# Kernel optimization log

Measured on AMD Instinct MI355X. Metric: run time of the kernel, lower is better.

The kernel has to match this reference:

```python
import jax, jax.numpy as jnp
import numpy as np

B, S, DMODEL, NHEAD = 2, 2048, 1024, 16
DK = DMODEL // NHEAD
INITRANGE = 0.1


def setup_inputs() -> dict:
    key = jax.random.key(0)
    kq, kk, kv, kwq, kwk, kwv, kwo = jax.random.split(key, 7)
    unif = lambda k, shape: jax.random.uniform(k, shape, jnp.float32, -INITRANGE, INITRANGE)
    return {
        "Q": jax.random.normal(kq, (B, S, DMODEL), jnp.float32),
        "K": jax.random.normal(kk, (B, S, DMODEL), jnp.float32),
        "V": jax.random.normal(kv, (B, S, DMODEL), jnp.float32),
        "WQ": unif(kwq, (NHEAD, DMODEL, DK)),
        "WK": unif(kwk, (NHEAD, DMODEL, DK)),
        "WV": unif(kwv, (NHEAD, DMODEL, DK)),
        "WO": unif(kwo, (NHEAD * DK, DMODEL)),
    }


def reference(Q, K, V, WQ, WK, WV, WO):
    dk = WQ.shape[-1]
    # per-head projections: [B,S,D] x [H,D,dk] -> [B,H,S,dk]
    Qi = jnp.einsum('bsd,hdk->bhsk', Q, WQ)
    Ki = jnp.einsum('bsd,hdk->bhsk', K, WK)
    Vi = jnp.einsum('bsd,hdk->bhsk', V, WV)
    scale = 1.0 / jnp.sqrt(jnp.asarray(dk, Qi.dtype))
    # full attention matrix [B,H,S,S] (faithful to the hand-rolled module; dropout in eval mode)
    attn = jax.nn.softmax(jnp.einsum('bhsk,bhtk->bhst', Qi, Ki) * scale, axis=-1)
    headi = jnp.einsum('bhst,bhtk->bhsk', attn, Vi)  # [B,H,S,dk]
    b, h, s, _ = headi.shape
    # NOTE: original does a raw reshape of contiguous (B,H,S,dk) -> (B,S,H*dk),
    # which mixes head and sequence axes in memory order. jnp row-major reshape
    # reproduces exactly the same element layout.
    out = headi.reshape(b, s, h * dk) @ WO  # [B,S,DMODEL]
    return out
```

## Files before the change

kernel.cpp:

```cpp
#include <hip/hip_runtime.h>
#include <hip/hip_bf16.h>
#include <stdint.h>

typedef unsigned short u16;
typedef unsigned int u32;
typedef __attribute__((ext_vector_type(4))) float f32x4;
typedef __attribute__((ext_vector_type(16))) float f32x16;
typedef __attribute__((ext_vector_type(8))) short bf16x8;
typedef __attribute__((ext_vector_type(4))) unsigned int u32x4;
typedef __attribute__((ext_vector_type(2))) unsigned int u32x2;

#define DEV __device__ __forceinline__

DEV u16 f2bf(float f) {
  union { float f; uint32_t u; } v; v.f = f;
  uint32_t u = v.u;
  return (u16)((u + 0x7fffu + ((u >> 16) & 1u)) >> 16);
}
DEV float bf2f(u16 h) {
  union { uint32_t u; float f; } v; v.u = ((uint32_t)h) << 16;
  return v.f;
}

DEV u32 cvtpk(float a, float b) {
  u32 r;
  asm("v_cvt_pk_bf16_f32 %0, %1, %2" : "=v"(r) : "v"(a), "v"(b));
  return r;
}

DEV void gload_lds16(const u16* g, u16* l) {
  __builtin_amdgcn_global_load_lds(
      (const __attribute__((address_space(1))) void*)g,
      (__attribute__((address_space(3))) void*)l, 16, 0, 0);
}

__global__ __launch_bounds__(256) void prep_kernel(
    const float* __restrict__ Q, const float* __restrict__ K, const float* __restrict__ V,
    const float* __restrict__ WQ, const float* __restrict__ WK, const float* __restrict__ WV,
    const float* __restrict__ WO,
    u16* __restrict__ Qb, u16* __restrict__ Kb, u16* __restrict__ Vb,
    u16* __restrict__ Wt, u16* __restrict__ Wot) {
  const int i = blockIdx.x * 256 + threadIdx.x;
#pragma unroll
  for (int it = 0; it < 3; ++it) {
    int idx = it * 1048576 + i;
    int which = idx >> 20, j = idx & 1048575;
    const float* src = which == 0 ? Q : (which == 1 ? K : V);
    u16* dst = which == 0 ? Qb : (which == 1 ? Kb : Vb);
    float4 v = ((const float4*)src)[j];
    u32x2 pk;
    pk[0] = (u32)f2bf(v.x) | ((u32)f2bf(v.y) << 16);
    pk[1] = (u32)f2bf(v.z) | ((u32)f2bf(v.w) << 16);
    *(u32x2*)(dst + (size_t)j * 4) = pk;
  }
#pragma unroll
  for (int it = 0; it < 4; ++it) {
    int idx = it * 1048576 + i;
    if (idx < 3145728) {
      int p = idx >> 20, r = idx & 1048575;
      int n = r >> 10, d = r & 1023;
      int h = n >> 6, k = n & 63;
      const float* src = p == 0 ? WQ : (p == 1 ? WK : WV);
      Wt[idx] = f2bf(src[(h * 1024 + d) * 64 + k]);
    } else {
      int j = idx - 3145728;
      int c = j >> 10, k = j & 1023;
      Wot[j] = f2bf(WO[k * 1024 + c]);
    }
  }
}

template <int OUT_BF16>
__global__ __launch_bounds__(256, 2) void gemm_kernel(const u16* __restrict__ A,
                                                      const u16* __restrict__ Bt,
                                                      void* __restrict__ Cout) {
  __shared__ __align__(16) u16 Alds[128 * 64];
  __shared__ __align__(16) u16 Blds[128 * 64];
  const size_t zo = blockIdx.z;
  A += zo * 4194304;
  Bt += zo * 1048576;
  const int tid = threadIdx.x;
  const int l = tid & 63, w = tid >> 6;
  const int wm = w >> 1, wn = w & 1;
  const int tileM = blockIdx.x * 128, tileN = blockIdx.y * 128;
  const int lr = l >> 3, lch = l & 7;

  f32x4 acc[4][4] = {};

  for (int kt = 0; kt < 16; ++kt) {
    const int k0 = kt * 64;
#pragma unroll
    for (int i = 0; i < 4; ++i) {
      int r = i * 32 + w * 8 + lr;
      int sch = lch ^ (r & 7);
      gload_lds16(A + (size_t)(tileM + r) * 1024 + k0 + sch * 8, Alds + i * 2048 + w * 512);
      gload_lds16(Bt + (size_t)(tileN + r) * 1024 + k0 + sch * 8, Blds + i * 2048 + w * 512);
    }
    __syncthreads();
    bf16x8 af[4][2], bfr[4][2];
#pragma unroll
    for (int m = 0; m < 4; ++m) {
#pragma unroll
      for (int kk = 0; kk < 2; ++kk) {
        int row = wm * 64 + m * 16 + (l & 15);
        int ch = ((l >> 4) + kk * 4) ^ (row & 7);
        af[m][kk] = *(const bf16x8*)(Alds + row * 64 + ch * 8);
        int rowb = wn * 64 + m * 16 + (l & 15);
        int chb = ((l >> 4) + kk * 4) ^ (rowb & 7);
        bfr[m][kk] = *(const bf16x8*)(Blds + rowb * 64 + chb * 8);
      }
    }
#pragma unroll
    for (int m = 0; m < 4; ++m)
#pragma unroll
      for (int n = 0; n < 4; ++n)
#pragma unroll
        for (int kk = 0; kk < 2; ++kk)
          acc[m][n] = __builtin_amdgcn_mfma_f32_16x16x32_bf16(af[m][kk], bfr[n][kk], acc[m][n], 0, 0, 0);
    __syncthreads();
  }
#pragma unroll
  for (int m = 0; m < 4; ++m) {
    int row0 = tileM + wm * 64 + m * 16 + ((l >> 4) << 2);
#pragma unroll
    for (int n = 0; n < 4; ++n) {
      int col = tileN + wn * 64 + n * 16 + (l & 15);
#pragma unroll
      for (int q = 0; q < 4; ++q) {
        if (OUT_BF16)
          ((u16*)Cout)[zo * 4194304 + (size_t)(row0 + q) * 1024 + col] = f2bf(acc[m][n][q]);
        else
          ((float*)Cout)[(size_t)(row0 + q) * 1024 + col] = acc[m][n][q];
      }
    }
  }
}

__global__ __launch_bounds__(256) void transposeV_kernel(const u16* __restrict__ Vi,
                                                         u16* __restrict__ Vt) {
  __shared__ __align__(16) u16 tl[64][72];
  const int tid = threadIdx.x;
  const int st = blockIdx.x * 64;
  const int bh = blockIdx.y;
  const int b = bh >> 4, h = bh & 15;
#pragma unroll
  for (int i = 0; i < 2; ++i) {
    int idx = i * 256 + tid;
    int s = idx >> 3, ch = idx & 7;
    const u16* src = Vi + (size_t)(b * 2048 + st + s) * 1024 + h * 64 + ch * 8;
    u32x2 a = *(const u32x2*)src;
    u32x2 bb = *(const u32x2*)(src + 4);
    *(u32x2*)&tl[s][ch * 8] = a;
    *(u32x2*)&tl[s][ch * 8 + 4] = bb;
  }
  __syncthreads();
#pragma unroll
  for (int i = 0; i < 2; ++i) {
    int idx = i * 256 + tid;
    int dk = idx >> 3, ch = idx & 7;
    u32x4 outv;
    u16* tp = (u16*)&outv;
#pragma unroll
    for (int j = 0; j < 8; ++j) tp[j] = tl[ch * 8 + j][dk];
    *(u32x4*)(Vt + ((size_t)bh * 64 + dk) * 2048 + st + ch * 8) = outv;
  }
}

__global__ __launch_bounds__(256, 3) void attn_kernel(const u16* __restrict__ Qi,
                                                      const u16* __restrict__ Ki,
                                                      const u16* __restrict__ Vt,
                                                      u16* __restrict__ Op,
                                                      float* __restrict__ Lp) {
  __shared__ __align__(16) u16 Kl[2][4096];
  __shared__ __align__(16) u16 Vl[2][4096];
  const int tid = threadIdx.x;
  const int l = tid & 63, w = tid >> 6;
  const int lq = l & 31, hi = l >> 5;
  const int lr = l >> 3, lch = l & 7;
  const int dd = blockIdx.x;
  const int orig = (dd & 7) * 128 + (dd >> 3);
  const int bh = orig >> 5;
  const int rem = orig & 31;
  const int qb = rem >> 1, kvh = rem & 1;
  const int b = bh >> 4, h = bh & 15;
  const int qt = qb * 128 + w * 32;
  const int tb = kvh * 1024;

  const u16* Kbase = Ki + (size_t)b * 2048 * 1024 + h * 64;
  const u16* Vbase = Vt + (size_t)bh * 64 * 2048;

  bf16x8 qf[4];
  {
    const u16* qp = Qi + (size_t)(b * 2048 + qt + lq) * 1024 + h * 64 + hi * 8;
#pragma unroll
    for (int s = 0; s < 4; ++s) {
      u32x4 t4 = *(const u32x4*)(qp + s * 16);
      u16* tp = (u16*)&t4;
#pragma unroll
      for (int j = 0; j < 8; ++j) tp[j] = f2bf(bf2f(tp[j]) * 0.1803368867f);
      qf[s] = *(bf16x8*)&t4;
    }
  }

  f32x16 o0 = {}, o1 = {};
  float l_r = 0.f;

  auto STAGE = [&](int bb, int t) {
#pragma unroll
    for (int i = 0; i < 2; ++i) {
      int r = i * 32 + w * 8 + lr;
      int sch = lch ^ (r & 7);
      gload_lds16(Kbase + (size_t)(b ? 0 : 0, (size_t)(tb + t * 64 + r)) * 1024 + sch * 8,
                  Kl[bb] + i * 2048 + w * 512);
      gload_lds16(Vbase + (size_t)r * 2048 + tb + t * 64 + sch * 8,
                  Vl[bb] + i * 2048 + w * 512);
    }
  };

  STAGE(0, 0);

  for (int tile = 0; tile < 16; ++tile) {
    const int cur = tile & 1;
    __syncthreads();
    if (tile + 1 < 16) STAGE(cur ^ 1, tile + 1);
    const u16* kl = Kl[cur];
    const u16* vl = Vl[cur];

    f32x16 s0 = {}, s1 = {};
    __builtin_amdgcn_s_setprio(1);
#pragma unroll
    for (int s = 0; s < 4; ++s) {
      int row = lq, c = s * 2 + hi;
      bf16x8 kf = *(const bf16x8*)(kl + row * 64 + (c ^ (row & 7)) * 8);
      s0 = __builtin_amdgcn_mfma_f32_32x32x16_bf16(kf, qf[s], s0, 0, 0, 0);
    }
#pragma unroll
    for (int s = 0; s < 4; ++s) {
      int row = 32 + lq, c = s * 2 + hi;
      bf16x8 kf = *(const bf16x8*)(kl + row * 64 + (c ^ (row & 7)) * 8);
      s1 = __builtin_amdgcn_mfma_f32_32x32x16_bf16(kf, qf[s], s1, 0, 0, 0);
    }
    __builtin_amdgcn_s_setprio(0);

    float rs = 0.f;
    bf16x8 pa[4];
#pragma unroll
    for (int s4 = 0; s4 < 4; ++s4) {
      const int rb = 8 * (s4 & 1);
      float p[8];
#pragma unroll
      for (int j = 0; j < 8; ++j) {
        float sv = (s4 < 2) ? ((const float*)&s0)[rb + j] : ((const float*)&s1)[rb + j];
        p[j] = exp2f(sv);
        rs += p[j];
      }
      u32 w10 = cvtpk(p[0], p[1]);
      u32 w11 = cvtpk(p[2], p[3]);
      u32 w20 = cvtpk(p[4], p[5]);
      u32 w21 = cvtpk(p[6], p[7]);
      u32 send0 = hi ? w10 : w20, send1 = hi ? w11 : w21;
      u32 recv0 = __shfl_xor(send0, 32, 64);
      u32 recv1 = __shfl_xor(send1, 32, 64);
      u32x4 af;
      af[0] = hi ? recv0 : w10;
      af[1] = hi ? recv1 : w11;
      af[2] = hi ? w20 : recv0;
      af[3] = hi ? w21 : recv1;
      pa[s4] = *(bf16x8*)&af;
    }
    rs += __shfl_xor(rs, 32, 64);
    l_r += rs;

    __builtin_amdgcn_s_setprio(1);
#pragma unroll
    for (int s4 = 0; s4 < 4; ++s4) {
      int rowd = lq, c = s4 * 2 + hi;
      bf16x8 vf = *(const bf16x8*)(vl + rowd * 64 + (c ^ (rowd & 7)) * 8);
      o0 = __builtin_amdgcn_mfma_f32_32x32x16_bf16(pa[s4], vf, o0, 0, 0, 0);
    }
#pragma unroll
    for (int s4 = 0; s4 < 4; ++s4) {
      int rowd = 32 + lq, c = s4 * 2 + hi;
      bf16x8 vf = *(const bf16x8*)(vl + rowd * 64 + (c ^ (rowd & 7)) * 8);
      o1 = __builtin_amdgcn_mfma_f32_32x32x16_bf16(pa[s4], vf, o1, 0, 0, 0);
    }
    __builtin_amdgcn_s_setprio(0);
  }

#pragma unroll
  for (int r = 0; r < 16; ++r) {
    int qr = (r & 3) + 8 * (r >> 2) + 4 * hi;
    u16* hp = Op + (size_t)kvh * 4194304 + ((size_t)bh * 2048 + qt + qr) * 64;
    hp[lq] = f2bf(o0[r]);
    hp[32 + lq] = f2bf(o1[r]);
  }
  if (hi == 0) Lp[(size_t)kvh * 65536 + (size_t)bh * 2048 + qt + lq] = l_r;
}

__global__ __launch_bounds__(256) void combine_kernel(const u16* __restrict__ Op,
                                                      const float* __restrict__ Lp,
                                                      u16* __restrict__ Hd) {
  const int idx = blockIdx.x * 256 + threadIdx.x;
  const int g = idx >> 3, j = idx & 7;
  const float fac = 1.f / (Lp[g] + Lp[65536 + g]);
  const u16* a = Op + (size_t)g * 64 + j * 8;
  const u16* bptr = a + 4194304;
  u32x4 va = *(const u32x4*)a;
  u32x4 vb = *(const u32x4*)bptr;
  const u16* pa = (const u16*)&va;
  const u16* pb = (const u16*)&vb;
  u32x4 outv;
  u16* po = (u16*)&outv;
#pragma unroll
  for (int e = 0; e < 8; ++e) po[e] = f2bf((bf2f(pa[e]) + bf2f(pb[e])) * fac);
  *(u32x4*)(Hd + (size_t)g * 64 + j * 8) = outv;
}

extern "C" void kernel_launch(void* const* d_in, const int* in_sizes, int n_in,
                              void* d_out, int out_size, void* d_ws, size_t ws_size,
                              hipStream_t stream) {
  const float* Q = (const float*)d_in[0];
  const float* K = (const float*)d_in[1];
  const float* V = (const float*)d_in[2];
  const float* WQ = (const float*)d_in[3];
  const float* WK = (const float*)d_in[4];
  const float* WV = (const float*)d_in[5];
  const float* WO = (const float*)d_in[6];
  float* out = (float*)d_out;

  size_t off = 0;
  char* ws = (char*)d_ws;
  auto nxt = [&](size_t n) { void* p = ws + off; off += (n + 255) & ~(size_t)255; return p; };
  u16* Qb = (u16*)nxt(3ull * 4096 * 1024 * 2);
  u16* Qi = (u16*)nxt(3ull * 4096 * 1024 * 2);
  u16* Vtb = (u16*)nxt(4096ull * 1024 * 2);
  u16* Hd = (u16*)nxt(4096ull * 1024 * 2);
  u16* Wt = (u16*)nxt(3ull * 1048576 * 2);
  u16* Wot = (u16*)nxt(1048576ull * 2);
  u16* Ki = Qi + 4194304;
  u16* Vi = Qi + 2 * 4194304;
  u16* Op = Qb;
  float* Lp = (float*)(Qb + 2ull * 4194304);

  prep_kernel<<<4096, 256, 0, stream>>>(Q, K, V, WQ, WK, WV, WO, Qb, Qb + 4194304,
                                        Qb + 2 * 4194304, Wt, Wot);

  gemm_kernel<1><<<dim3(32, 8, 3), 256, 0, stream>>>(Qb, Wt, Qi);

  transposeV_kernel<<<dim3(32, 32), 256, 0, stream>>>(Vi, Vtb);

  attn_kernel<<<1024, 256, 0, stream>>>(Qi, Ki, Vtb, Op, Lp);

  combine_kernel<<<2048, 256, 0, stream>>>(Op, Lp, Hd);

  gemm_kernel<0><<<dim3(32, 8, 1), 256, 0, stream>>>(Hd, Wot, out);
}
```

Before: 154.0 us.

## Swap shuffles for permlane32 swap and compute row sums via MFMA with ones

```diff
diff --git a/kernel.cpp b/kernel.cpp
--- a/kernel.cpp
+++ b/kernel.cpp
@@ -26,6 +26,10 @@
   u32 r;
   asm("v_cvt_pk_bf16_f32 %0, %1, %2" : "=v"(r) : "v"(a), "v"(b));
   return r;
+}
+
+DEV void plswap(u32& a, u32& b) {
+  asm("v_permlane32_swap_b32 %0, %1" : "+v"(a), "+v"(b));
 }
 
 DEV void gload_lds16(const u16* g, u16* l) {
@@ -202,15 +206,21 @@
     }
   }
 
-  f32x16 o0 = {}, o1 = {};
-  float l_r = 0.f;
+  bf16x8 ones;
+  {
+    u32x4 ov;
+    ov[0] = ov[1] = ov[2] = ov[3] = 0x3F803F80u;
+    ones = *(bf16x8*)&ov;
+  }
+
+  f32x16 o0 = {}, o1 = {}, lacc = {};
 
   auto STAGE = [&](int bb, int t) {
 #pragma unroll
     for (int i = 0; i < 2; ++i) {
       int r = i * 32 + w * 8 + lr;
       int sch = lch ^ (r & 7);
-      gload_lds16(Kbase + (size_t)(b ? 0 : 0, (size_t)(tb + t * 64 + r)) * 1024 + sch * 8,
+      gload_lds16(Kbase + (size_t)(tb + t * 64 + r) * 1024 + sch * 8,
                   Kl[bb] + i * 2048 + w * 512);
       gload_lds16(Vbase + (size_t)r * 2048 + tb + t * 64 + sch * 8,
                   Vl[bb] + i * 2048 + w * 512);
@@ -219,6 +229,7 @@
 
   STAGE(0, 0);
 
+#pragma unroll 2
   for (int tile = 0; tile < 16; ++tile) {
     const int cur = tile & 1;
     __syncthreads();
@@ -242,7 +253,6 @@
     }
     __builtin_amdgcn_s_setprio(0);
 
-    float rs = 0.f;
     bf16x8 pa[4];
 #pragma unroll
     for (int s4 = 0; s4 < 4; ++s4) {
@@ -252,24 +262,20 @@
       for (int j = 0; j < 8; ++j) {
         float sv = (s4 < 2) ? ((const float*)&s0)[rb + j] : ((const float*)&s1)[rb + j];
         p[j] = exp2f(sv);
-        rs += p[j];
       }
       u32 w10 = cvtpk(p[0], p[1]);
       u32 w11 = cvtpk(p[2], p[3]);
       u32 w20 = cvtpk(p[4], p[5]);
       u32 w21 = cvtpk(p[6], p[7]);
-      u32 send0 = hi ? w10 : w20, send1 = hi ? w11 : w21;
-      u32 recv0 = __shfl_xor(send0, 32, 64);
-      u32 recv1 = __shfl_xor(send1, 32, 64);
+      plswap(w10, w20);
+      plswap(w11, w21);
       u32x4 af;
-      af[0] = hi ? recv0 : w10;
-      af[1] = hi ? recv1 : w11;
-      af[2] = hi ? w20 : recv0;
-      af[3] = hi ? w21 : recv1;
+      af[0] = w10;
+      af[1] = w11;
+      af[2] = w20;
+      af[3] = w21;
       pa[s4] = *(bf16x8*)&af;
     }
-    rs += __shfl_xor(rs, 32, 64);
-    l_r += rs;
 
     __builtin_amdgcn_s_setprio(1);
 #pragma unroll
@@ -284,6 +290,9 @@
       bf16x8 vf = *(const bf16x8*)(vl + rowd * 64 + (c ^ (rowd & 7)) * 8);
       o1 = __builtin_amdgcn_mfma_f32_32x32x16_bf16(pa[s4], vf, o1, 0, 0, 0);
     }
+#pragma unroll
+    for (int s4 = 0; s4 < 4; ++s4)
+      lacc = __builtin_amdgcn_mfma_f32_32x32x16_bf16(pa[s4], ones, lacc, 0, 0, 0);
     __builtin_amdgcn_s_setprio(0);
   }
 
@@ -294,7 +303,13 @@
     hp[lq] = f2bf(o0[r]);
     hp[32 + lq] = f2bf(o1[r]);
   }
-  if (hi == 0) Lp[(size_t)kvh * 65536 + (size_t)bh * 2048 + qt + lq] = l_r;
+  if (lq == 0) {
+#pragma unroll
+    for (int r = 0; r < 16; ++r) {
+      int qr = (r & 3) + 8 * (r >> 2) + 4 * hi;
+      Lp[(size_t)kvh * 65536 + (size_t)bh * 2048 + qt + qr] = lacc[r];
+    }
+  }
 }
 
 __global__ __launch_bounds__(256) void combine_kernel(const u16* __restrict__ Op,
```

Result: no change. 154.1 us (+0.1%).
